# Optimization experiments

Measured on AMD Instinct MI355X. Metric: run time of the kernel, lower is better.

## Reference

```python
import jax, jax.numpy as jnp
import numpy as np

B, DQ, DKV, T, A, H, O = 131072, 13, 32, 24, 32, 4, 32
HD = A // H  # head_dim = 8
LN_EPS = 1e-5


def setup_inputs() -> dict:
    key = jax.random.key(0)
    ks = jax.random.split(key, 9)
    s = 0.1
    return {
        "query": jax.random.normal(ks[0], (B, DQ), dtype=jnp.float32),
        "kv": jax.random.normal(ks[1], (B, T, DKV), dtype=jnp.float32),
        "Wq": jax.random.normal(ks[2], (DQ, A), dtype=jnp.float32) * s,
        "Wk": jax.random.normal(ks[3], (DKV, A), dtype=jnp.float32) * s,
        "Wv": jax.random.normal(ks[4], (DKV, A), dtype=jnp.float32) * s,
        "Wo": jax.random.normal(ks[5], (A, O), dtype=jnp.float32) * s,
        "ln_w": jnp.ones((O,), dtype=jnp.float32),
        "ln_b": jnp.zeros((O,), dtype=jnp.float32),
        "Wd1": jax.random.normal(ks[6], (O, O), dtype=jnp.float32) * s,
        "Wd2": jax.random.normal(ks[7], (O, O), dtype=jnp.float32) * s,
    }


def reference(query, kv, Wq, Wk, Wv, Wo, ln_w, ln_b, Wd1, Wd2):
    # projections (Linear, no bias)
    q = query @ Wq                    # [B, A]
    k = jnp.einsum('btd,da->bta', kv, Wk)  # [B, T, A]
    v = jnp.einsum('btd,da->bta', kv, Wv)  # [B, T, A]
    # split heads: single query token -> [B, H, HD]
    qh = q.reshape(B, H, HD)
    kh = k.reshape(B, T, H, HD)
    vh = v.reshape(B, T, H, HD)
    scale = jnp.asarray(np.sqrt(HD), dtype=q.dtype)
    scores = jnp.einsum('bhd,bthd->bht', qh, kh) / scale  # [B, H, T]
    attn = jax.nn.softmax(scores, axis=-1)
    ctx = jnp.einsum('bht,bthd->bhd', attn, vh).reshape(B, A)
    out = ctx @ Wo                    # [B, O]
    # LayerNorm over last dim
    mu = jnp.mean(out, axis=-1, keepdims=True)
    var = jnp.mean(jnp.square(out - mu), axis=-1, keepdims=True)
    out = (out - mu) * jax.lax.rsqrt(var + LN_EPS) * ln_w + ln_b
    # residual GELU MLP (two Linear+GELU blocks), exact erf GELU like torch
    h = jax.nn.gelu(out @ Wd1, approximate=False)
    h = jax.nn.gelu(h @ Wd2, approximate=False)
    return out + h
```

## Files before the change

### kernel.cpp

```cpp
#include <hip/hip_runtime.h>
#include <hip/hip_bf16.h>

#define LN_EPS 1e-5f

typedef __attribute__((ext_vector_type(8))) short short8;
typedef __attribute__((ext_vector_type(4))) float float4v;
typedef __attribute__((ext_vector_type(2))) unsigned int uint2v;

__device__ __forceinline__ short f2bf(float f) {
    union { __hip_bfloat16 h; short s; } u; u.h = __float2bfloat16(f); return u.s;
}
__device__ __forceinline__ float bfbits2f(unsigned short v) {
    return __uint_as_float(((unsigned int)v) << 16);
}
__device__ __forceinline__ void split8(const float* x, short8& hi, short8& lo) {
    #pragma unroll
    for (int j = 0; j < 8; ++j) {
        short h = f2bf(x[j]);
        hi[j] = h;
        lo[j] = f2bf(x[j] - bfbits2f((unsigned short)h));
    }
}
__device__ __forceinline__ uint2v pack4(float4v v) {
    unsigned a = ((unsigned)(unsigned short)f2bf(v[0])) | (((unsigned)(unsigned short)f2bf(v[1])) << 16);
    unsigned b = ((unsigned)(unsigned short)f2bf(v[2])) | (((unsigned)(unsigned short)f2bf(v[3])) << 16);
    uint2v r; r[0] = a; r[1] = b; return r;
}
__device__ __forceinline__ float dot4(uint2v a, uint2v v) {
    float s;
    s  = __uint_as_float(a[0] << 16)          * __uint_as_float(v[0] << 16);
    s += __uint_as_float(a[0] & 0xffff0000u)  * __uint_as_float(v[0] & 0xffff0000u);
    s += __uint_as_float(a[1] << 16)          * __uint_as_float(v[1] << 16);
    s += __uint_as_float(a[1] & 0xffff0000u)  * __uint_as_float(v[1] & 0xffff0000u);
    return s;
}
__device__ __forceinline__ float gelu_exact(float x) {
    return 0.5f * x * (1.0f + erff(x * 0.70710678118654752440f));
}

__global__ __launch_bounds__(256, 3)
void cross_dmha_fused(const float* __restrict__ query,
                      const float* __restrict__ kv,
                      const float* __restrict__ Wq,
                      const float* __restrict__ Wk,
                      const float* __restrict__ Wv,
                      const float* __restrict__ Wo,
                      const float* __restrict__ lnw,
                      const float* __restrict__ lnb,
                      const float* __restrict__ Wd1,
                      const float* __restrict__ Wd2,
                      float* __restrict__ out)
{
    __shared__ __align__(16) float s_q  [4][4 * 36];
    __shared__ __align__(16) short s_qe [4][4 * 136];
    __shared__ __align__(16) float s_sc [4][4 * 144];
    __shared__ __align__(16) short s_at [4][4 * 160];
    __shared__ __align__(16) float s_ctx[4][4 * 36];
    __shared__ __align__(16) float s_y  [4][4 * 36];

    const int tid = threadIdx.x;
    const int l = tid & 63;
    const int w = tid >> 6;
    const int lm = l & 15;
    const int quad = l >> 4;
    const int E0 = blockIdx.x * 16 + w * 4;

    float* sq  = s_q[w];  short* sqe = s_qe[w];
    float* ssc = s_sc[w]; short* sat = s_at[w];
    float* sctx = s_ctx[w]; float* sy = s_y[w];

    const float4v z = {0.f, 0.f, 0.f, 0.f};

    short8 wv0, wv1, woh0, wol0, woh1, wol1, wd1a, wd1b, wd2a, wd2b;
    #pragma unroll
    for (int j = 0; j < 8; ++j) {
        int k8 = quad * 8 + j;
        wv0[j] = f2bf(Wv[k8 * 32 + lm]);
        wv1[j] = f2bf(Wv[k8 * 32 + 16 + lm]);
        float wo0 = Wo[k8 * 32 + lm], wo1 = Wo[k8 * 32 + 16 + lm];
        short h0 = f2bf(wo0); woh0[j] = h0; wol0[j] = f2bf(wo0 - bfbits2f((unsigned short)h0));
        short h1 = f2bf(wo1); woh1[j] = h1; wol1[j] = f2bf(wo1 - bfbits2f((unsigned short)h1));
        wd1a[j] = f2bf(Wd1[k8 * 32 + lm]);
        wd1b[j] = f2bf(Wd1[k8 * 32 + 16 + lm]);
        wd2a[j] = f2bf(Wd2[k8 * 32 + lm]);
        wd2b[j] = f2bf(Wd2[k8 * 32 + 16 + lm]);
    }

    {
        int e = quad;
        const float* qr = query + (size_t)(E0 + e) * 13;
        float a0 = 0.f, a1 = 0.f;
        #pragma unroll
        for (int d = 0; d < 13; ++d) {
            float qq = qr[d];
            a0 += qq * Wq[d * 32 + lm];
            a1 += qq * Wq[d * 32 + 16 + lm];
        }
        sq[e * 36 + lm] = a0;
        sq[e * 36 + 16 + lm] = a1;
    }
    __syncthreads();

    {
        int e = quad, h = lm >> 2, D0 = (lm & 3) * 8;
        float4v q0 = *(const float4v*)&sq[e * 36 + h * 8];
        float4v q1 = *(const float4v*)&sq[e * 36 + h * 8 + 4];
        short8 p;
        #pragma unroll
        for (int Di = 0; Di < 8; ++Di) {
            const float* wr = Wk + (D0 + Di) * 32 + h * 8;
            float4v k0 = *(const float4v*)wr;
            float4v k1 = *(const float4v*)(wr + 4);
            float acc = q0[0]*k0[0] + q0[1]*k0[1] + q0[2]*k0[2] + q0[3]*k0[3]
                      + q1[0]*k1[0] + q1[1]*k1[1] + q1[2]*k1[2] + q1[3]*k1[3];
            p[Di] = f2bf(acc * 0.35355339059327373f);
        }
        *(short8*)&sqe[e * 136 + lm * 8] = p;
    }
    __syncthreads();

    uint2v vpk[4][4];
    #pragma unroll
    for (int e = 0; e < 4; ++e) {
        short8 qf = {0,0,0,0,0,0,0,0};
        if (lm < 4) qf = *(const short8*)&sqe[e * 136 + lm * 32 + quad * 8];

        const float* kvb = kv + (size_t)(E0 + e) * 24 * 32 + quad * 8;
        float x0[8];
        {
            const float* src = kvb + lm * 32;
            float4v f0 = *(const float4v*)src, f1 = *(const float4v*)(src + 4);
            x0[0]=f0[0]; x0[1]=f0[1]; x0[2]=f0[2]; x0[3]=f0[3];
            x0[4]=f1[0]; x0[5]=f1[1]; x0[6]=f1[2]; x0[7]=f1[3];
        }
        float x1[8] = {0,0,0,0,0,0,0,0};
        if (lm < 8) {
            const float* src = kvb + (16 + lm) * 32;
            float4v f0 = *(const float4v*)src, f1 = *(const float4v*)(src + 4);
            x1[0]=f0[0]; x1[1]=f0[1]; x1[2]=f0[2]; x1[3]=f0[3];
            x1[4]=f1[0]; x1[5]=f1[1]; x1[6]=f1[2]; x1[7]=f1[3];
        }
        short8 ah0, al0, ah1, al1;
        split8(x0, ah0, al0);
        split8(x1, ah1, al1);

        float4v v00 = __builtin_amdgcn_mfma_f32_16x16x32_bf16(al0, wv0, z, 0, 0, 0);
        v00 = __builtin_amdgcn_mfma_f32_16x16x32_bf16(ah0, wv0, v00, 0, 0, 0);
        float4v v01 = __builtin_amdgcn_mfma_f32_16x16x32_bf16(al0, wv1, z, 0, 0, 0);
        v01 = __builtin_amdgcn_mfma_f32_16x16x32_bf16(ah0, wv1, v01, 0, 0, 0);
        float4v v10 = __builtin_amdgcn_mfma_f32_16x16x32_bf16(al1, wv0, z, 0, 0, 0);
        v10 = __builtin_amdgcn_mfma_f32_16x16x32_bf16(ah1, wv0, v10, 0, 0, 0);
        float4v v11 = __builtin_amdgcn_mfma_f32_16x16x32_bf16(al1, wv1, z, 0, 0, 0);
        v11 = __builtin_amdgcn_mfma_f32_16x16x32_bf16(ah1, wv1, v11, 0, 0, 0);

        float4v sc0 = __builtin_amdgcn_mfma_f32_16x16x32_bf16(ah0, qf, z, 0, 0, 0);
        float4v sc1 = __builtin_amdgcn_mfma_f32_16x16x32_bf16(ah1, qf, z, 0, 0, 0);

        vpk[e][0] = pack4(v00);
        vpk[e][1] = pack4(v01);
        vpk[e][2] = pack4(v10);
        vpk[e][3] = pack4(v11);

        if (lm < 4) {
            *(float4v*)&ssc[e * 144 + lm * 36 + quad * 4] = sc0;
            if (quad < 2)
                *(float4v*)&ssc[e * 144 + lm * 36 + 16 + quad * 4] = sc1;
        }
    }
    __syncthreads();

    if (l < 16) {
        int e = l >> 2, h = l & 3;
        const float* sc = &ssc[e * 144 + h * 36];
        float4v r[6];
        #pragma unroll
        for (int b = 0; b < 6; ++b) r[b] = *(const float4v*)&sc[b * 4];
        float mx = -1e30f;
        #pragma unroll
        for (int b = 0; b < 6; ++b)
            #pragma unroll
            for (int i = 0; i < 4; ++i) mx = fmaxf(mx, r[b][i]);
        float ex[24]; float sum = 0.f;
        #pragma unroll
        for (int b = 0; b < 6; ++b)
            #pragma unroll
            for (int i = 0; i < 4; ++i) { float v = __expf(r[b][i] - mx); ex[b*4+i] = v; sum += v; }
        float inv = 1.f / sum;
        short8 p[4];
        #pragma unroll
        for (int t = 0; t < 24; ++t) p[t >> 3][t & 7] = f2bf(ex[t] * inv);
        #pragma unroll
        for (int t = 24; t < 32; ++t) p[t >> 3][t & 7] = 0;
        short* dst = &sat[e * 160 + h * 40];
        *(short8*)&dst[0]  = p[0];
        *(short8*)&dst[8]  = p[1];
        *(short8*)&dst[16] = p[2];
        *(short8*)&dst[24] = p[3];
    }
    __syncthreads();

    #pragma unroll
    for (int e = 0; e < 4; ++e) {
        int hA = lm >> 3, hB = 2 + (lm >> 3);
        uint2v a00 = *(const uint2v*)&sat[e * 160 + hA * 40 + quad * 4];
        uint2v a01 = *(const uint2v*)&sat[e * 160 + hB * 40 + quad * 4];
        uint2v a10 = *(const uint2v*)&sat[e * 160 + hA * 40 + 16 + quad * 4];
        uint2v a11 = *(const uint2v*)&sat[e * 160 + hB * 40 + 16 + quad * 4];
        float pc0 = dot4(a00, vpk[e][0]) + dot4(a10, vpk[e][2]);
        float pc1 = dot4(a01, vpk[e][1]) + dot4(a11, vpk[e][3]);
        pc0 += __shfl_xor(pc0, 16); pc0 += __shfl_xor(pc0, 32);
        pc1 += __shfl_xor(pc1, 16); pc1 += __shfl_xor(pc1, 32);
        if (l < 16) {
            sctx[e * 36 + lm] = pc0;
            sctx[e * 36 + 16 + lm] = pc1;
        }
    }
    __syncthreads();

    short8 cah = {0,0,0,0,0,0,0,0}, cal = {0,0,0,0,0,0,0,0};
    if (lm < 4) {
        float cx[8];
        float4v c0 = *(const float4v*)&sctx[lm * 36 + quad * 8];
        float4v c1 = *(const float4v*)&sctx[lm * 36 + quad * 8 + 4];
        cx[0]=c0[0]; cx[1]=c0[1]; cx[2]=c0[2]; cx[3]=c0[3];
        cx[4]=c1[0]; cx[5]=c1[1]; cx[6]=c1[2]; cx[7]=c1[3];
        split8(cx, cah, cal);
    }
    float4v o0 = __builtin_amdgcn_mfma_f32_16x16x32_bf16(cal, woh0, z, 0, 0, 0);
    o0 = __builtin_amdgcn_mfma_f32_16x16x32_bf16(cah, wol0, o0, 0, 0, 0);
    o0 = __builtin_amdgcn_mfma_f32_16x16x32_bf16(cah, woh0, o0, 0, 0, 0);
    float4v o1 = __builtin_amdgcn_mfma_f32_16x16x32_bf16(cal, woh1, z, 0, 0, 0);
    o1 = __builtin_amdgcn_mfma_f32_16x16x32_bf16(cah, wol1, o1, 0, 0, 0);
    o1 = __builtin_amdgcn_mfma_f32_16x16x32_bf16(cah, woh1, o1, 0, 0, 0);

    float lw0 = lnw[lm], lw1 = lnw[16 + lm], lb0 = lnb[lm], lb1 = lnb[16 + lm];
    float y0r[4], y1r[4];
    #pragma unroll
    for (int i = 0; i < 4; ++i) {
        float tot = o0[i] + o1[i];
        tot += __shfl_xor(tot, 1); tot += __shfl_xor(tot, 2);
        tot += __shfl_xor(tot, 4); tot += __shfl_xor(tot, 8);
        float mu = tot * (1.f / 32.f);
        float d0 = o0[i] - mu, d1 = o1[i] - mu;
        float sqs = d0 * d0 + d1 * d1;
        sqs += __shfl_xor(sqs, 1); sqs += __shfl_xor(sqs, 2);
        sqs += __shfl_xor(sqs, 4); sqs += __shfl_xor(sqs, 8);
        float rstd = rsqrtf(sqs * (1.f / 32.f) + LN_EPS);
        y0r[i] = d0 * rstd * lw0 + lb0;
        y1r[i] = d1 * rstd * lw1 + lb1;
    }
    if (l < 16) {
        #pragma unroll
        for (int i = 0; i < 4; ++i) { sy[i * 36 + lm] = y0r[i]; sy[i * 36 + 16 + lm] = y1r[i]; }
    }
    __syncthreads();

    short8 yah = {0,0,0,0,0,0,0,0}, yal = {0,0,0,0,0,0,0,0};
    if (lm < 4) {
        float yx[8];
        float4v a = *(const float4v*)&sy[lm * 36 + quad * 8];
        float4v b = *(const float4v*)&sy[lm * 36 + quad * 8 + 4];
        yx[0]=a[0]; yx[1]=a[1]; yx[2]=a[2]; yx[3]=a[3];
        yx[4]=b[0]; yx[5]=b[1]; yx[6]=b[2]; yx[7]=b[3];
        split8(yx, yah, yal);
    }
    float4v g0 = __builtin_amdgcn_mfma_f32_16x16x32_bf16(yal, wd1a, z, 0, 0, 0);
    g0 = __builtin_amdgcn_mfma_f32_16x16x32_bf16(yah, wd1a, g0, 0, 0, 0);
    float4v g1 = __builtin_amdgcn_mfma_f32_16x16x32_bf16(yal, wd1b, z, 0, 0, 0);
    g1 = __builtin_amdgcn_mfma_f32_16x16x32_bf16(yah, wd1b, g1, 0, 0, 0);
    float h0r[4], h1r[4];
    #pragma unroll
    for (int i = 0; i < 4; ++i) { h0r[i] = gelu_exact(g0[i]); h1r[i] = gelu_exact(g1[i]); }
    __syncthreads();
    if (l < 16) {
        #pragma unroll
        for (int i = 0; i < 4; ++i) { sy[i * 36 + lm] = h0r[i]; sy[i * 36 + 16 + lm] = h1r[i]; }
    }
    __syncthreads();

    short8 hah = {0,0,0,0,0,0,0,0}, hal = {0,0,0,0,0,0,0,0};
    if (lm < 4) {
        float hx[8];
        float4v a = *(const float4v*)&sy[lm * 36 + quad * 8];
        float4v b = *(const float4v*)&sy[lm * 36 + quad * 8 + 4];
        hx[0]=a[0]; hx[1]=a[1]; hx[2]=a[2]; hx[3]=a[3];
        hx[4]=b[0]; hx[5]=b[1]; hx[6]=b[2]; hx[7]=b[3];
        split8(hx, hah, hal);
    }
    float4v m0 = __builtin_amdgcn_mfma_f32_16x16x32_bf16(hal, wd2a, z, 0, 0, 0);
    m0 = __builtin_amdgcn_mfma_f32_16x16x32_bf16(hah, wd2a, m0, 0, 0, 0);
    float4v m1 = __builtin_amdgcn_mfma_f32_16x16x32_bf16(hal, wd2b, z, 0, 0, 0);
    m1 = __builtin_amdgcn_mfma_f32_16x16x32_bf16(hah, wd2b, m1, 0, 0, 0);

    if (l < 16) {
        #pragma unroll
        for (int i = 0; i < 4; ++i) {
            float f0 = y0r[i] + gelu_exact(m0[i]);
            float f1 = y1r[i] + gelu_exact(m1[i]);
            size_t ob = (size_t)(E0 + i) * 32;
            out[ob + lm] = f0;
            out[ob + 16 + lm] = f1;
        }
    }
}

extern "C" void kernel_launch(void* const* d_in, const int* in_sizes, int n_in,
                              void* d_out, int out_size, void* d_ws, size_t ws_size,
                              hipStream_t stream) {
    const float* query = (const float*)d_in[0];
    const float* kv    = (const float*)d_in[1];
    const float* Wq    = (const float*)d_in[2];
    const float* Wk    = (const float*)d_in[3];
    const float* Wv    = (const float*)d_in[4];
    const float* Wo    = (const float*)d_in[5];
    const float* ln_w  = (const float*)d_in[6];
    const float* ln_b  = (const float*)d_in[7];
    const float* Wd1   = (const float*)d_in[8];
    const float* Wd2   = (const float*)d_in[9];
    float* out = (float*)d_out;

    int B = in_sizes[0] / 13;
    int grid = B / 16;
    cross_dmha_fused<<<grid, 256, 0, stream>>>(
        query, kv, Wq, Wk, Wv, Wo, ln_w, ln_b, Wd1, Wd2, out);
}
```

Baseline: 599.9 us.

## Batch post-attention MLP in one wave, drop kv split precision, use wave-level syncs

Several changes land together. The K/V projection now uses a single bf16 term instead of the hi/lo split, which halves the MFMA work on kv at a cost in precision. Most block barriers become wave-local lgkmcnt waits. The output projection, LayerNorm and MLP for all 16 rows of a block now run in wave 0 using full 16-row MFMA tiles, while the other waves exit early. Weight loads for the tail stages move after the barrier so they are done by one wave only, and the occupancy hint rises to 4. Relying on s_waitcnt alone for intra-wave LDS visibility depends on lockstep execution, and the serialized tail in wave 0 may limit overlap.

Measured after the change: 563.8 us. 6.0% less time.

```diff
diff --git a/kernel.cpp b/kernel.cpp
--- a/kernel.cpp
+++ b/kernel.cpp
@@ -7,11 +7,27 @@
 typedef __attribute__((ext_vector_type(4))) float float4v;
 typedef __attribute__((ext_vector_type(2))) unsigned int uint2v;
 
+#define WAVE_SYNC() asm volatile("s_waitcnt lgkmcnt(0)" ::: "memory")
+
 __device__ __forceinline__ short f2bf(float f) {
     union { __hip_bfloat16 h; short s; } u; u.h = __float2bfloat16(f); return u.s;
 }
 __device__ __forceinline__ float bfbits2f(unsigned short v) {
     return __uint_as_float(((unsigned int)v) << 16);
+}
+__device__ __forceinline__ unsigned packpair(float a, float b) {
+    union { __hip_bfloat162 h2; unsigned u; } t;
+    t.h2 = __float22bfloat162_rn(make_float2(a, b));
+    return t.u;
+}
+__device__ __forceinline__ short8 cvt8(float4v a, float4v b) {
+    union { unsigned u; short s[2]; } t;
+    short8 r;
+    t.u = packpair(a[0], a[1]); r[0] = t.s[0]; r[1] = t.s[1];
+    t.u = packpair(a[2], a[3]); r[2] = t.s[0]; r[3] = t.s[1];
+    t.u = packpair(b[0], b[1]); r[4] = t.s[0]; r[5] = t.s[1];
+    t.u = packpair(b[2], b[3]); r[6] = t.s[0]; r[7] = t.s[1];
+    return r;
 }
 __device__ __forceinline__ void split8(const float* x, short8& hi, short8& lo) {
     #pragma unroll
@@ -22,23 +38,21 @@
     }
 }
 __device__ __forceinline__ uint2v pack4(float4v v) {
-    unsigned a = ((unsigned)(unsigned short)f2bf(v[0])) | (((unsigned)(unsigned short)f2bf(v[1])) << 16);
-    unsigned b = ((unsigned)(unsigned short)f2bf(v[2])) | (((unsigned)(unsigned short)f2bf(v[3])) << 16);
-    uint2v r; r[0] = a; r[1] = b; return r;
+    uint2v r; r[0] = packpair(v[0], v[1]); r[1] = packpair(v[2], v[3]); return r;
 }
 __device__ __forceinline__ float dot4(uint2v a, uint2v v) {
     float s;
-    s  = __uint_as_float(a[0] << 16)          * __uint_as_float(v[0] << 16);
-    s += __uint_as_float(a[0] & 0xffff0000u)  * __uint_as_float(v[0] & 0xffff0000u);
-    s += __uint_as_float(a[1] << 16)          * __uint_as_float(v[1] << 16);
-    s += __uint_as_float(a[1] & 0xffff0000u)  * __uint_as_float(v[1] & 0xffff0000u);
+    s  = __uint_as_float(a[0] << 16)         * __uint_as_float(v[0] << 16);
+    s += __uint_as_float(a[0] & 0xffff0000u) * __uint_as_float(v[0] & 0xffff0000u);
+    s += __uint_as_float(a[1] << 16)         * __uint_as_float(v[1] << 16);
+    s += __uint_as_float(a[1] & 0xffff0000u) * __uint_as_float(v[1] & 0xffff0000u);
     return s;
 }
 __device__ __forceinline__ float gelu_exact(float x) {
     return 0.5f * x * (1.0f + erff(x * 0.70710678118654752440f));
 }
 
-__global__ __launch_bounds__(256, 3)
+__global__ __launch_bounds__(256, 4)
 void cross_dmha_fused(const float* __restrict__ query,
                       const float* __restrict__ kv,
                       const float* __restrict__ Wq,
@@ -55,40 +69,31 @@
     __shared__ __align__(16) short s_qe [4][4 * 136];
     __shared__ __align__(16) float s_sc [4][4 * 144];
     __shared__ __align__(16) short s_at [4][4 * 160];
-    __shared__ __align__(16) float s_ctx[4][4 * 36];
-    __shared__ __align__(16) float s_y  [4][4 * 36];
+    __shared__ __align__(16) float s_ctxb[16 * 36];
+    __shared__ __align__(16) float s_yb  [16 * 36];
 
     const int tid = threadIdx.x;
     const int l = tid & 63;
     const int w = tid >> 6;
     const int lm = l & 15;
     const int quad = l >> 4;
-    const int E0 = blockIdx.x * 16 + w * 4;
-
-    float* sq  = s_q[w];  short* sqe = s_qe[w];
+    const int B0 = blockIdx.x * 16;
+    const int E0 = B0 + w * 4;
+
+    float* sq = s_q[w];  short* sqe = s_qe[w];
     float* ssc = s_sc[w]; short* sat = s_at[w];
-    float* sctx = s_ctx[w]; float* sy = s_y[w];
-
     const float4v z = {0.f, 0.f, 0.f, 0.f};
 
-    short8 wv0, wv1, woh0, wol0, woh1, wol1, wd1a, wd1b, wd2a, wd2b;
+    short8 wv0, wv1;
     #pragma unroll
     for (int j = 0; j < 8; ++j) {
         int k8 = quad * 8 + j;
         wv0[j] = f2bf(Wv[k8 * 32 + lm]);
         wv1[j] = f2bf(Wv[k8 * 32 + 16 + lm]);
-        float wo0 = Wo[k8 * 32 + lm], wo1 = Wo[k8 * 32 + 16 + lm];
-        short h0 = f2bf(wo0); woh0[j] = h0; wol0[j] = f2bf(wo0 - bfbits2f((unsigned short)h0));
-        short h1 = f2bf(wo1); woh1[j] = h1; wol1[j] = f2bf(wo1 - bfbits2f((unsigned short)h1));
-        wd1a[j] = f2bf(Wd1[k8 * 32 + lm]);
-        wd1b[j] = f2bf(Wd1[k8 * 32 + 16 + lm]);
-        wd2a[j] = f2bf(Wd2[k8 * 32 + lm]);
-        wd2b[j] = f2bf(Wd2[k8 * 32 + 16 + lm]);
-    }
-
-    {
-        int e = quad;
-        const float* qr = query + (size_t)(E0 + e) * 13;
+    }
+
+    {
+        const float* qr = query + (size_t)(E0 + quad) * 13;
         float a0 = 0.f, a1 = 0.f;
         #pragma unroll
         for (int d = 0; d < 13; ++d) {
@@ -96,15 +101,15 @@
             a0 += qq * Wq[d * 32 + lm];
             a1 += qq * Wq[d * 32 + 16 + lm];
         }
-        sq[e * 36 + lm] = a0;
-        sq[e * 36 + 16 + lm] = a1;
-    }
-    __syncthreads();
-
-    {
-        int e = quad, h = lm >> 2, D0 = (lm & 3) * 8;
-        float4v q0 = *(const float4v*)&sq[e * 36 + h * 8];
-        float4v q1 = *(const float4v*)&sq[e * 36 + h * 8 + 4];
+        sq[quad * 36 + lm] = a0;
+        sq[quad * 36 + 16 + lm] = a1;
+    }
+    WAVE_SYNC();
+
+    {
+        int h = lm >> 2, D0 = (lm & 3) * 8;
+        float4v q0 = *(const float4v*)&sq[quad * 36 + h * 8];
+        float4v q1 = *(const float4v*)&sq[quad * 36 + h * 8 + 4];
         short8 p;
         #pragma unroll
         for (int Di = 0; Di < 8; ++Di) {
@@ -115,9 +120,9 @@
                       + q1[0]*k1[0] + q1[1]*k1[1] + q1[2]*k1[2] + q1[3]*k1[3];
             p[Di] = f2bf(acc * 0.35355339059327373f);
         }
-        *(short8*)&sqe[e * 136 + lm * 8] = p;
-    }
-    __syncthreads();
+        *(short8*)&sqe[quad * 136 + lm * 8] = p;
+    }
+    WAVE_SYNC();
 
     uint2v vpk[4][4];
     #pragma unroll
@@ -125,34 +130,21 @@
         short8 qf = {0,0,0,0,0,0,0,0};
         if (lm < 4) qf = *(const short8*)&sqe[e * 136 + lm * 32 + quad * 8];
 
-        const float* kvb = kv + (size_t)(E0 + e) * 24 * 32 + quad * 8;
-        float x0[8];
-        {
-            const float* src = kvb + lm * 32;
-            float4v f0 = *(const float4v*)src, f1 = *(const float4v*)(src + 4);
-            x0[0]=f0[0]; x0[1]=f0[1]; x0[2]=f0[2]; x0[3]=f0[3];
-            x0[4]=f1[0]; x0[5]=f1[1]; x0[6]=f1[2]; x0[7]=f1[3];
-        }
-        float x1[8] = {0,0,0,0,0,0,0,0};
+        const float* kvb = kv + ((size_t)(E0 + e) * 24) * 32 + quad * 8;
+        float4v f0a = *(const float4v*)(kvb + lm * 32);
+        float4v f0b = *(const float4v*)(kvb + lm * 32 + 4);
+        float4v f1a = z, f1b = z;
         if (lm < 8) {
-            const float* src = kvb + (16 + lm) * 32;
-            float4v f0 = *(const float4v*)src, f1 = *(const float4v*)(src + 4);
-            x1[0]=f0[0]; x1[1]=f0[1]; x1[2]=f0[2]; x1[3]=f0[3];
-            x1[4]=f1[0]; x1[5]=f1[1]; x1[6]=f1[2]; x1[7]=f1[3];
-        }
-        short8 ah0, al0, ah1, al1;
-        split8(x0, ah0, al0);
-        split8(x1, ah1, al1);
-
-        float4v v00 = __builtin_amdgcn_mfma_f32_16x16x32_bf16(al0, wv0, z, 0, 0, 0);
-        v00 = __builtin_amdgcn_mfma_f32_16x16x32_bf16(ah0, wv0, v00, 0, 0, 0);
-        float4v v01 = __builtin_amdgcn_mfma_f32_16x16x32_bf16(al0, wv1, z, 0, 0, 0);
-        v01 = __builtin_amdgcn_mfma_f32_16x16x32_bf16(ah0, wv1, v01, 0, 0, 0);
-        float4v v10 = __builtin_amdgcn_mfma_f32_16x16x32_bf16(al1, wv0, z, 0, 0, 0);
-        v10 = __builtin_amdgcn_mfma_f32_16x16x32_bf16(ah1, wv0, v10, 0, 0, 0);
-        float4v v11 = __builtin_amdgcn_mfma_f32_16x16x32_bf16(al1, wv1, z, 0, 0, 0);
-        v11 = __builtin_amdgcn_mfma_f32_16x16x32_bf16(ah1, wv1, v11, 0, 0, 0);
-
+            f1a = *(const float4v*)(kvb + (16 + lm) * 32);
+            f1b = *(const float4v*)(kvb + (16 + lm) * 32 + 4);
+        }
+        short8 ah0 = cvt8(f0a, f0b);
+        short8 ah1 = cvt8(f1a, f1b);
+
+        float4v v00 = __builtin_amdgcn_mfma_f32_16x16x32_bf16(ah0, wv0, z, 0, 0, 0);
+        float4v v01 = __builtin_amdgcn_mfma_f32_16x16x32_bf16(ah0, wv1, z, 0, 0, 0);
+        float4v v10 = __builtin_amdgcn_mfma_f32_16x16x32_bf16(ah1, wv0, z, 0, 0, 0);
+        float4v v11 = __builtin_amdgcn_mfma_f32_16x16x32_bf16(ah1, wv1, z, 0, 0, 0);
         float4v sc0 = __builtin_amdgcn_mfma_f32_16x16x32_bf16(ah0, qf, z, 0, 0, 0);
         float4v sc1 = __builtin_amdgcn_mfma_f32_16x16x32_bf16(ah1, qf, z, 0, 0, 0);
 
@@ -167,7 +159,7 @@
                 *(float4v*)&ssc[e * 144 + lm * 36 + 16 + quad * 4] = sc1;
         }
     }
-    __syncthreads();
+    WAVE_SYNC();
 
     if (l < 16) {
         int e = l >> 2, h = l & 3;
@@ -197,11 +189,11 @@
         *(short8*)&dst[16] = p[2];
         *(short8*)&dst[24] = p[3];
     }
-    __syncthreads();
+    WAVE_SYNC();
 
     #pragma unroll
     for (int e = 0; e < 4; ++e) {
-        int hA = lm >> 3, hB = 2 + (lm >> 3);
+        int hA = lm >> 3, hB = 2 + hA;
         uint2v a00 = *(const uint2v*)&sat[e * 160 + hA * 40 + quad * 4];
         uint2v a01 = *(const uint2v*)&sat[e * 160 + hB * 40 + quad * 4];
         uint2v a10 = *(const uint2v*)&sat[e * 160 + hA * 40 + 16 + quad * 4];
@@ -211,21 +203,34 @@
         pc0 += __shfl_xor(pc0, 16); pc0 += __shfl_xor(pc0, 32);
         pc1 += __shfl_xor(pc1, 16); pc1 += __shfl_xor(pc1, 32);
         if (l < 16) {
-            sctx[e * 36 + lm] = pc0;
-            sctx[e * 36 + 16 + lm] = pc1;
+            s_ctxb[(w * 4 + e) * 36 + lm] = pc0;
+            s_ctxb[(w * 4 + e) * 36 + 16 + lm] = pc1;
         }
     }
     __syncthreads();
-
-    short8 cah = {0,0,0,0,0,0,0,0}, cal = {0,0,0,0,0,0,0,0};
-    if (lm < 4) {
-        float cx[8];
-        float4v c0 = *(const float4v*)&sctx[lm * 36 + quad * 8];
-        float4v c1 = *(const float4v*)&sctx[lm * 36 + quad * 8 + 4];
+    if (w != 0) return;
+
+    short8 woh0, wol0, woh1, wol1, wd1a, wd1b, wd2a, wd2b;
+    #pragma unroll
+    for (int j = 0; j < 8; ++j) {
+        int k8 = quad * 8 + j;
+        float wo0 = Wo[k8 * 32 + lm], wo1 = Wo[k8 * 32 + 16 + lm];
+        short h0 = f2bf(wo0); woh0[j] = h0; wol0[j] = f2bf(wo0 - bfbits2f((unsigned short)h0));
+        short h1 = f2bf(wo1); woh1[j] = h1; wol1[j] = f2bf(wo1 - bfbits2f((unsigned short)h1));
+        wd1a[j] = f2bf(Wd1[k8 * 32 + lm]);
+        wd1b[j] = f2bf(Wd1[k8 * 32 + 16 + lm]);
+        wd2a[j] = f2bf(Wd2[k8 * 32 + lm]);
+        wd2b[j] = f2bf(Wd2[k8 * 32 + 16 + lm]);
+    }
+
+    float cx[8];
+    {
+        float4v c0 = *(const float4v*)&s_ctxb[lm * 36 + quad * 8];
+        float4v c1 = *(const float4v*)&s_ctxb[lm * 36 + quad * 8 + 4];
         cx[0]=c0[0]; cx[1]=c0[1]; cx[2]=c0[2]; cx[3]=c0[3];
         cx[4]=c1[0]; cx[5]=c1[1]; cx[6]=c1[2]; cx[7]=c1[3];
-        split8(cx, cah, cal);
-    }
+    }
+    short8 cah, cal; split8(cx, cah, cal);
     float4v o0 = __builtin_amdgcn_mfma_f32_16x16x32_bf16(cal, woh0, z, 0, 0, 0);
     o0 = __builtin_amdgcn_mfma_f32_16x16x32_bf16(cah, wol0, o0, 0, 0, 0);
     o0 = __builtin_amdgcn_mfma_f32_16x16x32_bf16(cah, woh0, o0, 0, 0, 0);
@@ -249,21 +254,21 @@
         y0r[i] = d0 * rstd * lw0 + lb0;
         y1r[i] = d1 * rstd * lw1 + lb1;
     }
-    if (l < 16) {
-        #pragma unroll
-        for (int i = 0; i < 4; ++i) { sy[i * 36 + lm] = y0r[i]; sy[i * 36 + 16 + lm] = y1r[i]; }
-    }
-    __syncthreads();
-
-    short8 yah = {0,0,0,0,0,0,0,0}, yal = {0,0,0,0,0,0,0,0};
-    if (lm < 4) {
-        float yx[8];
-        float4v a = *(const float4v*)&sy[lm * 36 + quad * 8];
-        float4v b = *(const float4v*)&sy[lm * 36 + quad * 8 + 4];
+    #pragma unroll
+    for (int i = 0; i < 4; ++i) {
+        s_yb[(quad * 4 + i) * 36 + lm] = y0r[i];
+        s_yb[(quad * 4 + i) * 36 + 16 + lm] = y1r[i];
+    }
+    WAVE_SYNC();
+
+    float yx[8];
+    {
+        float4v a = *(const float4v*)&s_yb[lm * 36 + quad * 8];
+        float4v b = *(const float4v*)&s_yb[lm * 36 + quad * 8 + 4];
         yx[0]=a[0]; yx[1]=a[1]; yx[2]=a[2]; yx[3]=a[3];
         yx[4]=b[0]; yx[5]=b[1]; yx[6]=b[2]; yx[7]=b[3];
-        split8(yx, yah, yal);
-    }
+    }
+    short8 yah, yal; split8(yx, yah, yal);
     float4v g0 = __builtin_amdgcn_mfma_f32_16x16x32_bf16(yal, wd1a, z, 0, 0, 0);
     g0 = __builtin_amdgcn_mfma_f32_16x16x32_bf16(yah, wd1a, g0, 0, 0, 0);
     float4v g1 = __builtin_amdgcn_mfma_f32_16x16x32_bf16(yal, wd1b, z, 0, 0, 0);
@@ -271,36 +276,33 @@
     float h0r[4], h1r[4];
     #pragma unroll
     for (int i = 0; i < 4; ++i) { h0r[i] = gelu_exact(g0[i]); h1r[i] = gelu_exact(g1[i]); }
-    __syncthreads();
-    if (l < 16) {
-        #pragma unroll
-        for (int i = 0; i < 4; ++i) { sy[i * 36 + lm] = h0r[i]; sy[i * 36 + 16 + lm] = h1r[i]; }
-    }
-    __syncthreads();
-
-    short8 hah = {0,0,0,0,0,0,0,0}, hal = {0,0,0,0,0,0,0,0};
-    if (lm < 4) {
-        float hx[8];
-        float4v a = *(const float4v*)&sy[lm * 36 + quad * 8];
-        float4v b = *(const float4v*)&sy[lm * 36 + quad * 8 + 4];
+    #pragma unroll
+    for (int i = 0; i < 4; ++i) {
+        s_ctxb[(quad * 4 + i) * 36 + lm] = h0r[i];
+        s_ctxb[(quad * 4 + i) * 36 + 16 + lm] = h1r[i];
+    }
+    WAVE_SYNC();
+
+    float hx[8];
+    {
+        float4v a = *(const float4v*)&s_ctxb[lm * 36 + quad * 8];
+        float4v b = *(const float4v*)&s_ctxb[lm * 36 + quad * 8 + 4];
         hx[0]=a[0]; hx[1]=a[1]; hx[2]=a[2]; hx[3]=a[3];
         hx[4]=b[0]; hx[5]=b[1]; hx[6]=b[2]; hx[7]=b[3];
-        split8(hx, hah, hal);
-    }
+    }
+    short8 hah, hal; split8(hx, hah, hal);
     float4v m0 = __builtin_amdgcn_mfma_f32_16x16x32_bf16(hal, wd2a, z, 0, 0, 0);
     m0 = __builtin_amdgcn_mfma_f32_16x16x32_bf16(hah, wd2a, m0, 0, 0, 0);
     float4v m1 = __builtin_amdgcn_mfma_f32_16x16x32_bf16(hal, wd2b, z, 0, 0, 0);
     m1 = __builtin_amdgcn_mfma_f32_16x16x32_bf16(hah, wd2b, m1, 0, 0, 0);
 
-    if (l < 16) {
-        #pragma unroll
-        for (int i = 0; i < 4; ++i) {
-            float f0 = y0r[i] + gelu_exact(m0[i]);
-            float f1 = y1r[i] + gelu_exact(m1[i]);
-            size_t ob = (size_t)(E0 + i) * 32;
-            out[ob + lm] = f0;
-            out[ob + 16 + lm] = f1;
-        }
+    #pragma unroll
+    for (int i = 0; i < 4; ++i) {
+        float f0 = y0r[i] + gelu_exact(m0[i]);
+        float f1 = y1r[i] + gelu_exact(m1[i]);
+        size_t ob = (size_t)(B0 + quad * 4 + i) * 32;
+        out[ob + lm] = f0;
+        out[ob + 16 + lm] = f1;
     }
 }
 
```
